# Kernel optimization log

Hardware: AMD Instinct MI355X
Metric: run time of the kernel (lower is better)

The kernel has to match this reference:

```python
import jax, jax.numpy as jnp
import numpy as np

_S = np.float32(1.0 / np.sqrt(2.0))
_lo = np.array([_S, _S], np.float32)   # dec_lo reversed == rec_lo for db1
_hi = np.array([_S, -_S], np.float32)  # dec_hi reversed == rec_hi for db1
# filters[k][i,j]: k=0 LL/2, k=1 hi(i)*lo(j), k=2 lo(i)*hi(j), k=3 hi*hi  (matches torch unsqueeze outer products)
DEC = np.stack([np.outer(_lo, _lo) / 2.0, np.outer(_hi, _lo), np.outer(_lo, _hi), np.outer(_hi, _hi)]).astype(np.float32)
INV = np.stack([np.outer(_lo, _lo) * 2.0, np.outer(_hi, _lo), np.outer(_lo, _hi), np.outer(_hi, _hi)]).astype(np.float32)
INV_FLIP = np.ascontiguousarray(INV[:, ::-1, ::-1])  # spatially flipped for conv_transpose-as-dilated-conv

DN = ('NCHW', 'OIHW', 'NCHW')


def wt(x):
    # single grouped (depthwise x4) strided conv == per-channel loop in the original
    N, C, H, W = x.shape
    k = jnp.broadcast_to(jnp.asarray(DEC)[None], (C, 4, 2, 2)).reshape(C * 4, 1, 2, 2)
    r = jax.lax.conv_general_dilated(x, k, (2, 2), 'VALID', dimension_numbers=DN, feature_group_count=C)
    r = r.reshape(N, C, 4, H // 2, W // 2)
    r = jnp.concatenate([r[:, :, :1], (r[:, :, 1:] + 1.0) / 2.0], axis=2)  # detail remap
    return r.reshape(N, 4 * C, H // 2, W // 2)


def iwt(v):
    N, C4, H, W = v.shape
    C = C4 // 4
    r = v.reshape(N, C, 4, H, W)
    r = jnp.concatenate([r[:, :, :1], 2.0 * r[:, :, 1:] - 1.0], axis=2).reshape(N, C4, H, W)
    k = jnp.broadcast_to(jnp.asarray(INV_FLIP)[None], (C, 4, 2, 2))
    # conv_transpose2d(stride=2, k=2) == dilated conv with lhs_dilation=2, pad 1, flipped kernel
    return jax.lax.conv_general_dilated(r, k, (1, 1), ((1, 1), (1, 1)), lhs_dilation=(2, 2),
                                        dimension_numbers=DN, feature_group_count=C)


def ws_conv(x, w, b, pad):
    # weight standardization: subtract mean over (in,kh,kw), divide by per-filter std (unbiased) + 1e-5
    wc = w - w.mean(axis=(1, 2, 3), keepdims=True)
    std = wc.reshape(w.shape[0], -1).std(axis=1, ddof=1).reshape(-1, 1, 1, 1) + 1e-5
    y = jax.lax.conv_general_dilated(x, wc / std, (1, 1), ((pad, pad), (pad, pad)), dimension_numbers=DN)
    return y if b is None else y + b[None, :, None, None]


def gn(x, g, b, G):
    N, C, H, W = x.shape
    xr = x.reshape(N, G, -1)
    m = xr.mean(-1, keepdims=True)
    v = xr.var(-1, keepdims=True)
    xr = (xr - m) * jax.lax.rsqrt(v + 1e-5)
    return xr.reshape(N, C, H, W) * g[None, :, None, None] + b[None, :, None, None]


def lrelu(t):
    return jnp.where(t > 0, t, 0.2 * t)


def setup_inputs() -> dict:
    key = jax.random.key(0)
    ks = iter(jax.random.split(key, 32))
    f32 = jnp.float32
    d = {}
    d['x'] = jax.random.normal(next(ks), (16, 3, 256, 256), f32)
    def wgt(shape):
        return 0.05 * jax.random.normal(next(ks), shape, f32)
    def bias(n):
        return 0.01 * jax.random.normal(next(ks), (n,), f32)
    c = 16
    d['conv1_w'], d['conv1_b'] = wgt((c, 12, 3, 3)), bias(c)
    d['conv2_w'], d['conv2_b'] = wgt((4 * c, 4 * c, 3, 3)), bias(4 * c)
    d['conv3_w'], d['conv3_b'] = wgt((16 * c, 16 * c, 3, 3)), bias(16 * c)
    d['conv4_w'], d['conv4_b'] = wgt((64 * c, 64 * c, 3, 3)), bias(64 * c)
    d['convd1_w'], d['convd1_b'] = wgt((12, c, 3, 3)), bias(12)
    d['convd2_w'], d['convd2_b'] = wgt((c, 2 * c, 3, 3)), bias(c)
    d['convd3_w'], d['convd3_b'] = wgt((4 * c, 8 * c, 3, 3)), bias(4 * c)
    d['convd4_w'], d['convd4_b'] = wgt((16 * c, 32 * c, 3, 3)), bias(16 * c)
    d['final_w'] = wgt((2, 3, 1, 1))
    for name, n in (('gn1', c), ('gn2', 4 * c), ('gn3', 16 * c), ('gn4', 64 * c)):
        d[name + '_w'] = 1.0 + 0.1 * jax.random.normal(next(ks), (n,), f32)
        d[name + '_b'] = 0.01 * jax.random.normal(next(ks), (n,), f32)
    return d


def reference(x, conv1_w, conv1_b, conv2_w, conv2_b, conv3_w, conv3_b, conv4_w, conv4_b,
              convd1_w, convd1_b, convd2_w, convd2_b, convd3_w, convd3_b, convd4_w, convd4_b,
              final_w, gn1_w, gn1_b, gn2_w, gn2_b, gn3_w, gn3_b, gn4_w, gn4_b):
    w1 = wt(x)
    c1 = gn(lrelu(ws_conv(w1, conv1_w, conv1_b, 1)), gn1_w, gn1_b, 2)
    w2 = wt(c1)
    c2 = gn(lrelu(ws_conv(w2, conv2_w, conv2_b, 1)), gn2_w, gn2_b, 8)
    w3 = wt(c2)
    c3 = gn(lrelu(ws_conv(w3, conv3_w, conv3_b, 1)), gn3_w, gn3_b, 32)
    w4 = wt(c3)
    c4 = gn(lrelu(ws_conv(w4, conv4_w, conv4_b, 1)), gn4_w, gn4_b, 128)
    c5 = gn(lrelu(ws_conv(c4, conv4_w, conv4_b, 1)), gn4_w, gn4_b, 128)
    c6 = ws_conv(c5, conv4_w, conv4_b, 1)
    ic4 = lrelu(c6 + w4)
    iw4 = jnp.concatenate([c3, iwt(ic4)], axis=1)
    ic3 = gn(lrelu(ws_conv(iw4, convd4_w, convd4_b, 1)), gn3_w, gn3_b, 32)
    iw3 = jnp.concatenate([c2, iwt(ic3)], axis=1)
    ic2 = gn(lrelu(ws_conv(iw3, convd3_w, convd3_b, 1)), gn2_w, gn2_b, 8)
    iw2 = jnp.concatenate([c1, iwt(ic2)], axis=1)
    ic1 = gn(lrelu(ws_conv(iw2, convd2_w, convd2_b, 1)), gn1_w, gn1_b, 2)
    iw1 = lrelu(ws_conv(ic1, convd1_w, convd1_b, 1))
    y = ws_conv(iwt(iw1), final_w, None, 0)
    return y
```

## Files before the change

### kernel.cpp

```cpp
#include <hip/hip_runtime.h>
#include <math.h>


#define NB 16

typedef _Float16 f16;
typedef _Float16 f16x8 __attribute__((ext_vector_type(8)));
typedef _Float16 f16x4 __attribute__((ext_vector_type(4)));
typedef float f32x4 __attribute__((ext_vector_type(4)));
typedef unsigned int u32;

#define LLDS16(gp, lp)                                                          \
  __builtin_amdgcn_global_load_lds((const __attribute__((address_space(1))) u32*)(const void*)(gp), \
                                   (__attribute__((address_space(3))) u32*)(void*)(lp), 16, 0, 0)

__device__ __forceinline__ void ws_reduce(const float* wp, int fan, float* red,
                                          float& mean, float& inv) {
  float s = 0.f, s2 = 0.f;
  for (int i = threadIdx.x; i < fan; i += 256) { float v = wp[i]; s += v; s2 += v * v; }
  red[threadIdx.x] = s; red[256 + threadIdx.x] = s2;
  __syncthreads();
  for (int st = 128; st > 0; st >>= 1) {
    if (threadIdx.x < st) {
      red[threadIdx.x] += red[threadIdx.x + st];
      red[256 + threadIdx.x] += red[256 + threadIdx.x + st];
    }
    __syncthreads();
  }
  float sum = red[0], sumsq = red[256];
  mean = sum / (float)fan;
  float var = (sumsq - sum * mean) / (float)(fan - 1);
  if (var < 0.f) var = 0.f;
  inv = 1.0f / (sqrtf(var) + 1e-5f);
}

__global__ void ws_all_kernel(const float* w0, float* o0, const float* w1, float* o1,
                              const float* w2, float* o2, const float* w3, float* o3) {
  __shared__ float red[512];
  int b = blockIdx.x;
  const float* w; float* o; int fan, oi;
  if (b < 16)      { w = w0; o = o0; fan = 108; oi = b; }
  else if (b < 28) { w = w1; o = o1; fan = 144; oi = b - 16; }
  else if (b < 44) { w = w2; o = o2; fan = 288; oi = b - 28; }
  else             { w = w3; o = o3; fan = 3;   oi = b - 44; }
  const float* wp = w + (size_t)oi * fan;
  float mean, inv; ws_reduce(wp, fan, red, mean, inv);
  for (int i = threadIdx.x; i < fan; i += 256)
    o[(size_t)oi * fan + i] = (wp[i] - mean) * inv;
}

__global__ void ws_f16_all_kernel(const float* w0, f16* o0, const float* w1, f16* o1,
                                  const float* w2, f16* o2, const float* w3, f16* o3,
                                  const float* w4, f16* o4) {
  __shared__ float red[512];
  int b = blockIdx.x;
  const float* w; f16* o; int fan, Cin, Cout, oi;
  if (b < 64)        { w = w0; o = o0; fan = 576;  Cin = 64;   Cout = 64;   oi = b; }
  else if (b < 320)  { w = w1; o = o1; fan = 2304; Cin = 256;  Cout = 256;  oi = b - 64; }
  else if (b < 1344) { w = w2; o = o2; fan = 9216; Cin = 1024; Cout = 1024; oi = b - 320; }
  else if (b < 1408) { w = w3; o = o3; fan = 1152; Cin = 128;  Cout = 64;   oi = b - 1344; }
  else               { w = w4; o = o4; fan = 4608; Cin = 512;  Cout = 256;  oi = b - 1408; }
  const float* wp = w + (size_t)oi * fan;
  float mean, inv; ws_reduce(wp, fan, red, mean, inv);
  for (int i = threadIdx.x; i < fan; i += 256) {
    int ci = i / 9, tap = i - ci * 9;
    o[((size_t)tap * Cout + oi) * Cin + ci] = (f16)((wp[i] - mean) * inv);
  }
}

__device__ __forceinline__ void halo_write(f16* buf, int C, int H, int W, int t) {
  int c8s = C >> 3;
  int c8 = t % c8s; int q = t / c8s;
  int P = 2 * (W + 2) + 2 * H;
  int b = q % P; int n = q / P;
  int y, x;
  if (b < W + 2) { y = 0; x = b; }
  else if (b < 2 * (W + 2)) { y = H + 1; x = b - (W + 2); }
  else { int bb = b - 2 * (W + 2); y = 1 + (bb >> 1); x = (bb & 1) ? (W + 1) : 0; }
  size_t a = (((size_t)n * (H + 2) + y) * (W + 2) + x) * C + c8 * 8;
  *(f16x8*)(buf + a) = (f16x8){0, 0, 0, 0, 0, 0, 0, 0};
}

__global__ void halo2_kernel(f16* b0, int c0, int h0, int w0, int n0,
                             f16* b1, int c1, int h1, int w1, int total) {
  int idx = blockIdx.x * 256 + threadIdx.x;
  if (idx >= total) return;
  if (idx < n0) halo_write(b0, c0, h0, w0, idx);
  else halo_write(b1, c1, h1, w1, idx - n0);
}

__global__ void zero_halo_kernel(f16* __restrict__ buf, int C, int H, int W, int total8) {
  int idx = blockIdx.x * 256 + threadIdx.x;
  if (idx >= total8) return;
  halo_write(buf, C, H, W, idx);
}

__global__ void wt_kernel(const float* __restrict__ in, float* __restrict__ out,
                          int C, int Ho, int Wo, int total) {
  int idx = blockIdx.x * 256 + threadIdx.x;
  if (idx >= total) return;
  int w = idx % Wo; int t = idx / Wo;
  int h = t % Ho; t /= Ho;
  int c = t % C; int n = t / C;
  int Wi = 2 * Wo;
  const float* ip = in + (((size_t)n * C + c) * (2 * Ho) + 2 * h) * Wi + 2 * w;
  float a = ip[0], b = ip[1], cc = ip[Wi], d = ip[Wi + 1];
  size_t cs = (size_t)Ho * Wo;
  float* op = out + (((size_t)n * 4 * C + 4 * c) * Ho + h) * Wo + w;
  op[0]      = 0.25f * (a + b + cc + d);
  op[cs]     = 0.25f * (a + b - cc - d) + 0.5f;
  op[2 * cs] = 0.25f * (a - b + cc - d) + 0.5f;
  op[3 * cs] = 0.25f * (a - b - cc + d) + 0.5f;
}

__global__ void concat_iwt_kernel(const float* __restrict__ skip, const float* __restrict__ v,
                                  float* __restrict__ out, const float* __restrict__ gnp,
                                  const float* __restrict__ gamma, const float* __restrict__ beta,
                                  int G, int Sg, int len, int C, int Hh, int Wh,
                                  int totalA, int total) {
  int idx = blockIdx.x * 256 + threadIdx.x;
  if (idx >= total) return;
  int W = 2 * Wh, H = 2 * Hh; int HWs = H * W;
  if (idx < totalA) {
    int p = idx % HWs; int t = idx / HWs; int c = t % C; int n = t / C;
    out[((size_t)n * 2 * C + c) * HWs + p] = skip[idx];
    return;
  }
  int i2 = idx - totalA;
  int w = i2 % Wh; int t = i2 / Wh; int h = t % Hh; t /= Hh;
  int c = t % C; int n = t / C;
  size_t cs = (size_t)Hh * Wh;
  const float* vp = v + (((size_t)n * 4 * C + 4 * c) * Hh + h) * Wh + w;
  float v0 = vp[0], v1 = vp[cs], v2 = vp[2 * cs], v3 = vp[3 * cs];
  if (gnp) {
    int cpg = (4 * C) / G;
    int g = (4 * c) / cpg;
    const float* pp = gnp + (size_t)((n * G + g) * Sg) * 2;
    float s = 0.f, s2 = 0.f;
    for (int i = 0; i < Sg; ++i) { s += pp[2 * i]; s2 += pp[2 * i + 1]; }
    float mean = s / (float)len;
    float var = s2 / (float)len - mean * mean;
    if (var < 0.f) var = 0.f;
    float inv = rsqrtf(var + 1e-5f);
    v0 = (v0 - mean) * inv * gamma[4 * c]     + beta[4 * c];
    v1 = (v1 - mean) * inv * gamma[4 * c + 1] + beta[4 * c + 1];
    v2 = (v2 - mean) * inv * gamma[4 * c + 2] + beta[4 * c + 2];
    v3 = (v3 - mean) * inv * gamma[4 * c + 3] + beta[4 * c + 3];
  }
  v1 = 2.f * v1 - 1.f; v2 = 2.f * v2 - 1.f; v3 = 2.f * v3 - 1.f;
  float* op = out + (((size_t)n * 2 * C + C + c) * H + 2 * h) * (size_t)W + 2 * w;
  op[0]     = v0 + 0.5f * ( v1 + v2 + v3);
  op[1]     = v0 + 0.5f * ( v1 - v2 - v3);
  op[W]     = v0 + 0.5f * (-v1 + v2 - v3);
  op[W + 1] = v0 + 0.5f * (-v1 - v2 + v3);
}

__global__ __launch_bounds__(256) void to_nhwc_pad_kernel(const float* __restrict__ in,
                                                          f16* __restrict__ out,
                                                          int C, int H, int W) {
  __shared__ f16 sm[32][264];
  int HW = H * W;
  int p0 = blockIdx.x * 256, c0 = blockIdx.y * 32, n = blockIdx.z;
  int t = threadIdx.x;
  const float* ip = in + ((size_t)n * C + c0) * HW + p0;
#pragma unroll 8
  for (int r = 0; r < 32; ++r) sm[r][t] = (f16)ip[(size_t)r * HW + t];
  __syncthreads();
#pragma unroll
  for (int i = 0; i < 4; ++i) {
    int c = t + i * 256;
    int pl = c >> 2, cio = (c & 3) * 8;
    f16x8 v;
#pragma unroll
    for (int u = 0; u < 8; ++u) v[u] = sm[cio + u][pl];
    int p = p0 + pl; int y = p / W; int x = p - y * W;
    *(f16x8*)(out + (((size_t)n * (H + 2) + y + 1) * (W + 2) + x + 1) * C + c0 + cio) = v;
  }
}

__global__ __launch_bounds__(256) void gn_nhwc_kernel(
    const float* __restrict__ in, const float* __restrict__ gnp,
    const float* __restrict__ gamma, const float* __restrict__ beta,
    f16* __restrict__ out, int C, int H, int W, int G, int Sg, int len) {
  __shared__ f16 sm[32][264];
  int HW = H * W;
  int p0 = blockIdx.x * 256, c0 = blockIdx.y * 32, n = blockIdx.z;
  int t = threadIdx.x;
  int cpg = C / G;
  const float* ip = in + ((size_t)n * C + c0) * HW + p0;
#pragma unroll 8
  for (int r = 0; r < 32; ++r) {
    int c = c0 + r; int g = c / cpg;
    const float* pp = gnp + (size_t)((n * G + g) * Sg) * 2;
    float s = 0.f, s2 = 0.f;
    for (int i = 0; i < Sg; ++i) { s += pp[2 * i]; s2 += pp[2 * i + 1]; }
    float mean = s / (float)len;
    float var = s2 / (float)len - mean * mean;
    if (var < 0.f) var = 0.f;
    float inv = rsqrtf(var + 1e-5f);
    float ga = gamma[c], be = beta[c];
    sm[r][t] = (f16)((ip[(size_t)r * HW + t] - mean) * inv * ga + be);
  }
  __syncthreads();
#pragma unroll
  for (int i = 0; i < 4; ++i) {
    int c = t + i * 256;
    int pl = c >> 2, cio = (c & 3) * 8;
    f16x8 v;
#pragma unroll
    for (int u = 0; u < 8; ++u) v[u] = sm[cio + u][pl];
    int p = p0 + pl; int y = p / W; int x = p - y * W;
    *(f16x8*)(out + (((size_t)n * (H + 2) + y + 1) * (W + 2) + x + 1) * C + c0 + cio) = v;
  }
}

__global__ void iwt_final_kernel(const float* __restrict__ v, const float* __restrict__ w,
                                 float* __restrict__ out, int total) {
  int idx = blockIdx.x * 256 + threadIdx.x;
  if (idx >= total) return;
  int ww = idx % 128; int t = idx / 128;
  int hh = t % 128; int n = t / 128;
  size_t cs = (size_t)128 * 128;
  float y0[3], y1[3], y2[3], y3[3];
#pragma unroll
  for (int c = 0; c < 3; ++c) {
    const float* vp = v + ((size_t)n * 12 + 4 * c) * cs + (size_t)hh * 128 + ww;
    float v0 = vp[0];
    float v1 = 2.f * vp[cs] - 1.f, v2 = 2.f * vp[2 * cs] - 1.f, v3 = 2.f * vp[3 * cs] - 1.f;
    y0[c] = v0 + 0.5f * ( v1 + v2 + v3);
    y1[c] = v0 + 0.5f * ( v1 - v2 - v3);
    y2[c] = v0 + 0.5f * (-v1 + v2 - v3);
    y3[c] = v0 + 0.5f * (-v1 - v2 + v3);
  }
  float w0 = w[0], w1 = w[1], w2 = w[2], w3 = w[3], w4 = w[4], w5 = w[5];
  size_t ocs = (size_t)256 * 256;
  float* o0 = out + (size_t)n * 2 * ocs + (size_t)(2 * hh) * 256 + 2 * ww;
  o0[0]   = w0 * y0[0] + w1 * y0[1] + w2 * y0[2];
  o0[1]   = w0 * y1[0] + w1 * y1[1] + w2 * y1[2];
  o0[256] = w0 * y2[0] + w1 * y2[1] + w2 * y2[2];
  o0[257] = w0 * y3[0] + w1 * y3[1] + w2 * y3[2];
  float* o1 = o0 + ocs;
  o1[0]   = w3 * y0[0] + w4 * y0[1] + w5 * y0[2];
  o1[1]   = w3 * y1[0] + w4 * y1[1] + w5 * y1[2];
  o1[256] = w3 * y2[0] + w4 * y2[1] + w5 * y2[2];
  o1[257] = w3 * y3[0] + w4 * y3[1] + w5 * y3[2];
}

__global__ __launch_bounds__(256) void conv_mfma6_kernel(
    const f16* __restrict__ A, const f16* __restrict__ Wp,
    f16* __restrict__ part, int Cin, int H, int W, int Cout, int HW) {
  constexpr int CH = 128 * 64;
  __shared__ f16 Asm[2 * CH];
  __shared__ f16 Bsm[2 * CH];

  const int tid = threadIdx.x;
  const int w = tid >> 6, lane = tid & 63;
  const int m0 = blockIdx.x * 128;
  const int co0 = blockIdx.y * 128;
  const int Wp2 = W + 2;

  const f16* gA[4]; const f16* gB[4];
  int lOff[4];
#pragma unroll
  for (int e = 0; e < 4; ++e) {
    int c = e * 256 + tid;
    int r = c >> 3, j = c & 7;
    int jx = j ^ (r & 7);
    int m = m0 + r; int n = m / HW; int p = m - n * HW;
    int y = p / W; int x = p - y * W;
    gA[e] = A + (((size_t)n * (H + 2) + y + 1) * Wp2 + (x + 1)) * Cin + jx * 8;
    gB[e] = Wp + (size_t)(co0 + r) * Cin + jx * 8;
    lOff[e] = (e * 256 + w * 64) * 8;
  }

  const int wm = w & 1, wn = w >> 1;
  const int lr = lane & 15, quad = lane >> 4;
  int aoffs[4][2], boffs[4][2];
#pragma unroll
  for (int i = 0; i < 4; ++i)
#pragma unroll
    for (int kk = 0; kk < 2; ++kk) {
      int r = wm * 64 + i * 16 + lr;
      int cidx = kk * 4 + quad;
      aoffs[i][kk] = (r * 8 + (cidx ^ (r & 7))) * 8;
      int rb = wn * 64 + i * 16 + lr;
      boffs[i][kk] = (rb * 8 + (cidx ^ (rb & 7))) * 8;
    }

  f32x4 acc[4][4];
#pragma unroll
  for (int i = 0; i < 4; ++i)
#pragma unroll
    for (int j = 0; j < 4; ++j) acc[i][j] = (f32x4){0.f, 0.f, 0.f, 0.f};

  const int kpt = Cin >> 6;
  const int nit = (9 * kpt) / gridDim.z;
  const int it0 = blockIdx.z * nit;
  const size_t bstride = (size_t)Cout * Cin;

  auto stageAB = [&](int it, int sel) {
    int tap = it / kpt, kk = it - tap * kpt;
    int dy = tap / 3 - 1, dx = tap % 3 - 1;
    long offA = ((long)dy * Wp2 + dx) * Cin + (kk << 6);
    long offB = (long)tap * bstride + (kk << 6);
    f16* ab = Asm + sel * CH;
    f16* bb = Bsm + sel * CH;
#pragma unroll
    for (int e = 0; e < 4; ++e) {
      LLDS16(gA[e] + offA, ab + lOff[e]);
      LLDS16(gB[e] + offB, bb + lOff[e]);
    }
  };

  stageAB(it0, 0);
  int sel = 0;
  for (int ii = 0; ii < nit; ++ii) {
    __syncthreads();
    if (ii + 1 < nit) stageAB(it0 + ii + 1, sel ^ 1);
    const f16* ab = Asm + sel * CH;
    const f16* bb = Bsm + sel * CH;
    f16x8 af[4][2], bf[4][2];
#pragma unroll
    for (int i = 0; i < 4; ++i)
#pragma unroll
      for (int kk = 0; kk < 2; ++kk) {
        af[i][kk] = *(const f16x8*)&ab[aoffs[i][kk]];
        bf[i][kk] = *(const f16x8*)&bb[boffs[i][kk]];
      }
#pragma unroll
    for (int kk = 0; kk < 2; ++kk)
#pragma unroll
      for (int i = 0; i < 4; ++i)
#pragma unroll
        for (int j = 0; j < 4; ++j)
          acc[i][j] = __builtin_amdgcn_mfma_f32_16x16x32_f16(af[i][kk], bf[j][kk], acc[i][j], 0, 0, 0);
    sel ^= 1;
  }

  const size_t pbase = (size_t)blockIdx.z * NB * Cout * HW;
#pragma unroll
  for (int i = 0; i < 4; ++i) {
    int mg = m0 + wm * 64 + i * 16 + quad * 4;
    int n = mg / HW, p = mg - n * HW;
#pragma unroll
    for (int j = 0; j < 4; ++j) {
      int co = co0 + wn * 64 + j * 16 + lr;
      f32x4 v = acc[i][j];
      f16x4 h;
#pragma unroll
      for (int r = 0; r < 4; ++r) h[r] = (f16)v[r];
      *(f16x4*)&part[pbase + ((size_t)n * Cout + co) * HW + p] = h;
    }
  }
}

__global__ __launch_bounds__(256) void reduceS_kernel(
    const f16* __restrict__ part, const float* __restrict__ bias,
    const float* __restrict__ add, float* __restrict__ out,
    int Cout, int HW, int S, int do_lrelu, int total4,
    float* __restrict__ gnp, int G, int Sg) {
  __shared__ float red[512];
  int idx = blockIdx.x * 256 + threadIdx.x;
  if (idx >= total4) return;
  size_t sstride = (size_t)NB * Cout * HW;
  int hw4 = HW >> 2;
  int p4 = idx % hw4; int t = idx / hw4;
  int c = t % Cout;
  size_t eoff = (size_t)t * HW + p4 * 4;
  float b = bias[c];
  f32x4 o = {b, b, b, b};
  for (int s = 0; s < S; ++s) {
    f16x4 a = *(const f16x4*)(part + s * sstride + eoff);
#pragma unroll
    for (int r = 0; r < 4; ++r) o[r] += (float)a[r];
  }
  if (add) {
    f32x4 av = *(const f32x4*)(add + eoff);
#pragma unroll
    for (int r = 0; r < 4; ++r) o[r] += av[r];
  }
  if (do_lrelu)
#pragma unroll
    for (int r = 0; r < 4; ++r) o[r] = o[r] > 0.f ? o[r] : 0.2f * o[r];
  *(f32x4*)(out + eoff) = o;
  if (gnp) {
    float ls = o[0] + o[1] + o[2] + o[3];
    float ls2 = o[0]*o[0] + o[1]*o[1] + o[2]*o[2] + o[3]*o[3];
    red[threadIdx.x] = ls; red[256 + threadIdx.x] = ls2;
    __syncthreads();
    for (int st = 128; st > 0; st >>= 1) {
      if (threadIdx.x < st) {
        red[threadIdx.x] += red[threadIdx.x + st];
        red[256 + threadIdx.x] += red[256 + threadIdx.x + st];
      }
      __syncthreads();
    }
    if (threadIdx.x == 0) {
      int flat0 = blockIdx.x * 1024;
      int chw = Cout * HW;
      int n = flat0 / chw;
      int rem = flat0 - n * chw;
      int L = (Cout / G) * HW;
      int g = rem / L;
      int s = (rem - g * L) >> 10;
      gnp[((n * G + g) * Sg + s) * 2] = red[0];
      gnp[((n * G + g) * Sg + s) * 2 + 1] = red[256];
    }
  }
}

__global__ __launch_bounds__(256) void conv_mfma2_kernel(
    const f16* __restrict__ A, const f16* __restrict__ Wp,
    const float* __restrict__ bias, float* __restrict__ out,
    int Cin, int H, int W, int Cout, int HW, int do_lrelu) {
  constexpr int BM = 128, BN = 64, BK = 64;
  __shared__ f16 Asm[BM * BK];
  __shared__ f16 Bsm[BN * BK];

  const int tid = threadIdx.x;
  const int w = tid >> 6, lane = tid & 63;
  const int m0 = blockIdx.x * BM;
  const int co0 = blockIdx.y * BN;
  const int Wp2 = W + 2;

  const f16* gA[4];
  int lAoff[4];
#pragma unroll
  for (int e = 0; e < 4; ++e) {
    int c = e * 256 + tid;
    int r = c >> 3, j = c & 7;
    int jx = j ^ (r & 7);
    int m = m0 + r; int n = m / HW; int p = m - n * HW;
    int y = p / W; int x = p - y * W;
    gA[e] = A + (((size_t)n * (H + 2) + y + 1) * Wp2 + (x + 1)) * Cin + jx * 8;
    lAoff[e] = (e * 256 + w * 64) * 8;
  }
  const f16* gB[2];
  int lBoff[2];
#pragma unroll
  for (int e = 0; e < 2; ++e) {
    int c = e * 256 + tid;
    int r = c >> 3, j = c & 7;
    int jx = j ^ (r & 7);
    gB[e] = Wp + (size_t)(co0 + r) * Cin + jx * 8;
    lBoff[e] = (e * 256 + w * 64) * 8;
  }

  const int wm = w & 1, wn = w >> 1;
  const int lr = lane & 15, quad = lane >> 4;
  int aoffs[4][2], boffs[2][2];
#pragma unroll
  for (int i = 0; i < 4; ++i)
#pragma unroll
    for (int kk = 0; kk < 2; ++kk) {
      int r = wm * 64 + i * 16 + lr;
      int cidx = kk * 4 + quad;
      aoffs[i][kk] = (r * 8 + (cidx ^ (r & 7))) * 8;
    }
#pragma unroll
  for (int jn = 0; jn < 2; ++jn)
#pragma unroll
    for (int kk = 0; kk < 2; ++kk) {
      int rb = wn * 32 + jn * 16 + lr;
      int cidx = kk * 4 + quad;
      boffs[jn][kk] = (rb * 8 + (cidx ^ (rb & 7))) * 8;
    }

  f32x4 acc[4][2];
#pragma unroll
  for (int i = 0; i < 4; ++i)
#pragma unroll
    for (int jn = 0; jn < 2; ++jn) acc[i][jn] = (f32x4){0.f, 0.f, 0.f, 0.f};

  for (int tap = 0; tap < 9; ++tap) {
    const int dy = tap / 3 - 1, dx = tap % 3 - 1;
    const long tapA = ((long)dy * Wp2 + dx) * Cin;
    const long tapB = (size_t)tap * Cout * Cin;
    for (int kc = 0; kc < Cin; kc += BK) {
      __syncthreads();
#pragma unroll
      for (int e = 0; e < 4; ++e) LLDS16(gA[e] + tapA + kc, Asm + lAoff[e]);
#pragma unroll
      for (int e = 0; e < 2; ++e) LLDS16(gB[e] + tapB + kc, Bsm + lBoff[e]);
      __syncthreads();

      f16x8 af[4][2], bf[2][2];
#pragma unroll
      for (int i = 0; i < 4; ++i)
#pragma unroll
        for (int kk = 0; kk < 2; ++kk) af[i][kk] = *(const f16x8*)&Asm[aoffs[i][kk]];
#pragma unroll
      for (int jn = 0; jn < 2; ++jn)
#pragma unroll
        for (int kk = 0; kk < 2; ++kk) bf[jn][kk] = *(const f16x8*)&Bsm[boffs[jn][kk]];
#pragma unroll
      for (int kk = 0; kk < 2; ++kk)
#pragma unroll
        for (int i = 0; i < 4; ++i)
#pragma unroll
          for (int jn = 0; jn < 2; ++jn)
            acc[i][jn] = __builtin_amdgcn_mfma_f32_16x16x32_f16(af[i][kk], bf[jn][kk], acc[i][jn], 0, 0, 0);
    }
  }

#pragma unroll
  for (int i = 0; i < 4; ++i) {
    int mg = m0 + wm * 64 + i * 16 + quad * 4;
    int n = mg / HW, p = mg - n * HW;
#pragma unroll
    for (int jn = 0; jn < 2; ++jn) {
      int co = co0 + wn * 32 + jn * 16 + lr;
      float b = bias[co];
      f32x4 v = acc[i][jn];
#pragma unroll
      for (int r = 0; r < 4; ++r) {
        float u = v[r] + b;
        v[r] = (do_lrelu && u < 0.f) ? 0.2f * u : u;
      }
      *(f32x4*)&out[((size_t)n * Cout + co) * HW + p] = v;
    }
  }
}

template <int CO, int CIC>
__global__ __launch_bounds__(256) void conv3x3_kernel(
    const float* __restrict__ in, const float* __restrict__ wgt,
    const float* __restrict__ bias, float* __restrict__ out,
    int Cin, int H, int W, int Cout, int do_lrelu, float* __restrict__ gnp) {
  __shared__ float sm[CIC][18][18];
  int tiles_x = W >> 4;
  int bt = blockIdx.x;
  int tx0 = (bt % tiles_x) << 4;
  int ty0 = (bt / tiles_x) << 4;
  int co0 = blockIdx.y * CO;
  int n = blockIdx.z;
  int tid = threadIdx.x;
  int lx = tid & 15, ly = tid >> 4;

  float acc[CO];
#pragma unroll
  for (int i = 0; i < CO; i++) acc[i] = 0.f;

  const float* inb = in + (size_t)n * Cin * H * W;

  for (int ci0 = 0; ci0 < Cin; ci0 += CIC) {
    __syncthreads();
    for (int idx = tid; idx < CIC * 324; idx += 256) {
      int ci = idx / 324;
      int r = idx - ci * 324;
      int gy = r / 18, gx = r - gy * 18;
      int iy = ty0 + gy - 1, ix = tx0 + gx - 1;
      float v = 0.f;
      if ((unsigned)iy < (unsigned)H && (unsigned)ix < (unsigned)W)
        v = inb[((size_t)(ci0 + ci)) * H * W + (size_t)iy * W + ix];
      sm[ci][gy][gx] = v;
    }
    __syncthreads();
#pragma unroll
    for (int ci = 0; ci < CIC; ci++) {
      float x00 = sm[ci][ly][lx],     x01 = sm[ci][ly][lx + 1],     x02 = sm[ci][ly][lx + 2];
      float x10 = sm[ci][ly + 1][lx], x11 = sm[ci][ly + 1][lx + 1], x12 = sm[ci][ly + 1][lx + 2];
      float x20 = sm[ci][ly + 2][lx], x21 = sm[ci][ly + 2][lx + 1], x22 = sm[ci][ly + 2][lx + 2];
      const float* wp = wgt + ((size_t)co0 * Cin + (ci0 + ci)) * 9;
#pragma unroll
      for (int co = 0; co < CO; co++) {
        const float* wc = wp + (size_t)co * Cin * 9;
        float a = acc[co];
        a = fmaf(wc[0], x00, a); a = fmaf(wc[1], x01, a); a = fmaf(wc[2], x02, a);
        a = fmaf(wc[3], x10, a); a = fmaf(wc[4], x11, a); a = fmaf(wc[5], x12, a);
        a = fmaf(wc[6], x20, a); a = fmaf(wc[7], x21, a); a = fmaf(wc[8], x22, a);
        acc[co] = a;
      }
    }
  }

  float vout[CO];
#pragma unroll
  for (int co = 0; co < CO; co++) {
    float v = acc[co] + bias[co0 + co];
    if (do_lrelu) v = v > 0.f ? v : 0.2f * v;
    vout[co] = v;
  }

  if (gnp) {
    float p0 = 0.f, q0 = 0.f, p1 = 0.f, q1 = 0.f;
#pragma unroll
    for (int co = 0; co < 8; ++co) { p0 += vout[co]; q0 += vout[co] * vout[co]; }
#pragma unroll
    for (int co = 8; co < CO; ++co) { p1 += vout[co]; q1 += vout[co] * vout[co]; }
    float* red = &sm[0][0][0];
    __syncthreads();
    red[tid] = p0; red[256 + tid] = q0; red[512 + tid] = p1; red[768 + tid] = q1;
    __syncthreads();
    for (int st = 128; st > 0; st >>= 1) {
      if (tid < st) {
        red[tid] += red[tid + st]; red[256 + tid] += red[256 + tid + st];
        red[512 + tid] += red[512 + tid + st]; red[768 + tid] += red[768 + tid + st];
      }
      __syncthreads();
    }
    if (tid == 0) {
      int S = gridDim.x;
      gnp[((n * 2 + 0) * S + blockIdx.x) * 2]     = red[0];
      gnp[((n * 2 + 0) * S + blockIdx.x) * 2 + 1] = red[256];
      gnp[((n * 2 + 1) * S + blockIdx.x) * 2]     = red[512];
      gnp[((n * 2 + 1) * S + blockIdx.x) * 2 + 1] = red[768];
    }
  }

  int oy = ty0 + ly, ox = tx0 + lx;
#pragma unroll
  for (int co = 0; co < CO; co++)
    out[(((size_t)n * Cout + co0 + co) * H + oy) * W + ox] = vout[co];
}

__global__ __launch_bounds__(256) void gn_stats_kernel(const float* __restrict__ x,
                                                       float* __restrict__ part,
                                                       int C, int HW, int G, int SPLIT) {
  __shared__ float red[512];
  int gs = blockIdx.x;
  int g = gs / SPLIT, s = gs - g * SPLIT;
  int n = blockIdx.y;
  int cpg = C / G;
  int len = cpg * HW;
  int chunk = len / SPLIT;
  size_t base = ((size_t)n * C + (size_t)g * cpg) * HW + (size_t)s * chunk;
  const f32x4* xp = (const f32x4*)(x + base);
  int chunk4 = chunk >> 2;
  float sm = 0.f, s2 = 0.f;
  for (int i = threadIdx.x; i < chunk4; i += 256) {
    f32x4 v = xp[i];
    sm += v.x + v.y + v.z + v.w;
    s2 += v.x * v.x + v.y * v.y + v.z * v.z + v.w * v.w;
  }
  red[threadIdx.x] = sm; red[256 + threadIdx.x] = s2;
  __syncthreads();
  for (int st = 128; st > 0; st >>= 1) {
    if (threadIdx.x < st) {
      red[threadIdx.x] += red[threadIdx.x + st];
      red[256 + threadIdx.x] += red[256 + threadIdx.x + st];
    }
    __syncthreads();
  }
  if (threadIdx.x == 0) {
    int o = ((n * G + g) * SPLIT + s) * 2;
    part[o] = red[0]; part[o + 1] = red[256];
  }
}

__global__ __launch_bounds__(256) void gn_apply_kernel(float* __restrict__ x,
                                                       const float* __restrict__ gnp,
                                                       const float* __restrict__ gamma,
                                                       const float* __restrict__ beta,
                                                       int C, int HW, int G, int Sg, int len,
                                                       int total4) {
  int idx = blockIdx.x * 256 + threadIdx.x;
  if (idx >= total4) return;
  int flat0 = blockIdx.x * 1024;
  int chw = C * HW;
  int n = flat0 / chw;
  int rem = flat0 - n * chw;
  int L = (C / G) * HW;
  int g = rem / L;
  const float* pp = gnp + (size_t)((n * G + g) * Sg) * 2;
  float s = 0.f, s2 = 0.f;
  for (int i = 0; i < Sg; ++i) { s += pp[2 * i]; s2 += pp[2 * i + 1]; }
  float mean = s / (float)len;
  float var = s2 / (float)len - mean * mean;
  if (var < 0.f) var = 0.f;
  float inv = rsqrtf(var + 1e-5f);
  int hw4 = HW >> 2;
  int p4 = idx % hw4; int t = idx / hw4;
  int c = t % C;
  float ga = gamma[c], be = beta[c];
  f32x4* xp = (f32x4*)(x + ((size_t)t * HW)) + p4;
  f32x4 v = *xp;
#pragma unroll
  for (int r = 0; r < 4; ++r) v[r] = (v[r] - mean) * inv * ga + be;
  *xp = v;
}


extern "C" void kernel_launch(void* const* d_in, const int* in_sizes, int n_in,
                              void* d_out, int out_size, void* d_ws, size_t ws_size,
                              hipStream_t stream) {
  const float* x        = (const float*)d_in[0];
  const float* conv1_w  = (const float*)d_in[1];
  const float* conv1_b  = (const float*)d_in[2];
  const float* conv2_w  = (const float*)d_in[3];
  const float* conv2_b  = (const float*)d_in[4];
  const float* conv3_w  = (const float*)d_in[5];
  const float* conv3_b  = (const float*)d_in[6];
  const float* conv4_w  = (const float*)d_in[7];
  const float* conv4_b  = (const float*)d_in[8];
  const float* convd1_w = (const float*)d_in[9];
  const float* convd1_b = (const float*)d_in[10];
  const float* convd2_w = (const float*)d_in[11];
  const float* convd2_b = (const float*)d_in[12];
  const float* convd3_w = (const float*)d_in[13];
  const float* convd3_b = (const float*)d_in[14];
  const float* convd4_w = (const float*)d_in[15];
  const float* convd4_b = (const float*)d_in[16];
  const float* final_w  = (const float*)d_in[17];
  const float* gn1_w = (const float*)d_in[18];
  const float* gn1_b = (const float*)d_in[19];
  const float* gn2_w = (const float*)d_in[20];
  const float* gn2_b = (const float*)d_in[21];
  const float* gn3_w = (const float*)d_in[22];
  const float* gn3_b = (const float*)d_in[23];
  const float* gn4_w = (const float*)d_in[24];
  const float* gn4_b = (const float*)d_in[25];

  char* base = (char*)d_ws;
  size_t off = 0;
  auto allocB = [&](size_t bytes) { size_t o = off; off = (off + bytes + 255) & ~(size_t)255; return o; };

  size_t o_sw1  = allocB(16 * 108 * 4);
  size_t o_swd1 = allocB(12 * 144 * 4);
  size_t o_swd2 = allocB(16 * 288 * 4);
  size_t o_swf  = allocB(6 * 4);
  size_t o_pw2  = allocB((size_t)9 * 64 * 64 * 2);
  size_t o_pw3  = allocB((size_t)9 * 256 * 256 * 2);
  size_t o_pw4  = allocB((size_t)9 * 1024 * 1024 * 2);
  size_t o_pwd3 = allocB((size_t)9 * 64 * 128 * 2);
  size_t o_pwd4 = allocB((size_t)9 * 256 * 512 * 2);
  size_t o_R1   = allocB((size_t)NB * 66 * 66 * 128 * 2);
  size_t o_R2   = allocB((size_t)NB * 34 * 34 * 512 * 2);
  size_t o_gnp  = allocB(16384 * 4);
  size_t o_c1 = allocB((size_t)NB * 16 * 128 * 128 * 4);
  size_t o_c2 = allocB((size_t)NB * 64 * 64 * 64 * 4);
  size_t o_c3 = allocB((size_t)NB * 256 * 32 * 32 * 4);
  size_t o_w4 = allocB((size_t)NB * 1024 * 16 * 16 * 4);
  size_t o_t1 = allocB((size_t)NB * 1024 * 16 * 16 * 4);
  size_t o_t2 = allocB((size_t)NB * 512 * 32 * 32 * 4);

  if (off > ws_size) return;

  float* c1 = (float*)(base + o_c1);
  float* c2 = (float*)(base + o_c2);
  float* c3 = (float*)(base + o_c3);
  float* w4 = (float*)(base + o_w4);
  float* t1 = (float*)(base + o_t1);
  float* t2 = (float*)(base + o_t2);
  f16* part  = (f16*)(base + o_R1);
  f16* ah64  = (f16*)(base + o_R1);
  f16* ah128 = (f16*)(base + o_R1);
  f16* ah256 = (f16*)(base + o_R2);
  f16* ah1k  = (f16*)(base + o_R2);
  f16* ah512 = (f16*)(base + o_R2);
  f16* pw2 = (f16*)(base + o_pw2);
  f16* pw3 = (f16*)(base + o_pw3);
  f16* pw4 = (f16*)(base + o_pw4);
  f16* pwd3 = (f16*)(base + o_pwd3);
  f16* pwd4 = (f16*)(base + o_pwd4);
  float* gnp = (float*)(base + o_gnp);

  {
    int n0 = NB * (2 * 66 + 2 * 64) * (64 / 8);
    int n1 = NB * (2 * 34 + 2 * 32) * (256 / 8);
    int tot = n0 + n1;
    halo2_kernel<<<(tot + 255) / 256, 256, 0, stream>>>(ah64, 64, 64, 64, n0,
                                                        ah256, 256, 32, 32, tot);
  }
  ws_all_kernel<<<46, 256, 0, stream>>>(conv1_w, (float*)(base + o_sw1),
                                        convd1_w, (float*)(base + o_swd1),
                                        convd2_w, (float*)(base + o_swd2),
                                        final_w, (float*)(base + o_swf));
  ws_f16_all_kernel<<<1664, 256, 0, stream>>>(conv2_w, pw2, conv3_w, pw3, conv4_w, pw4,
                                              convd3_w, pwd3, convd4_w, pwd4);

  auto prep_nhwc = [&](const float* in, f16* ah, int C, int H, int W, int zero) {
    if (zero) {
      int total8 = NB * (2 * (W + 2) + 2 * H) * (C / 8);
      zero_halo_kernel<<<(total8 + 255) / 256, 256, 0, stream>>>(ah, C, H, W, total8);
    }
    dim3 g((H * W) / 256, C / 32, NB);
    to_nhwc_pad_kernel<<<g, 256, 0, stream>>>(in, ah, C, H, W);
  };
  auto cm6 = [&](const f16* a, const f16* wt, const float* b, float* dest, const float* add,
                 int Cin, int Hs, int Ws, int Cout, int lr, int G, int Sg) {
    dim3 g((NB * Hs * Ws) / 128, Cout / 128, 2);
    conv_mfma6_kernel<<<g, 256, 0, stream>>>(a, wt, part, Cin, Hs, Ws, Cout, Hs * Ws);
    int total4 = (NB * Cout * Hs * Ws) >> 2;
    reduceS_kernel<<<(total4 + 255) / 256, 256, 0, stream>>>(
        part, b, add, dest, Cout, Hs * Ws, 2, lr, total4, G ? gnp : nullptr, G, Sg);
  };
  auto cm2 = [&](const f16* a, const f16* wt, const float* b, float* o,
                 int Cin, int Hs, int Ws, int Cout, int lr) {
    dim3 g((NB * Hs * Ws) / 128, Cout / 64);
    conv_mfma2_kernel<<<g, 256, 0, stream>>>(a, wt, b, o, Cin, Hs, Ws, Cout, Hs * Ws, lr);
  };
  auto launch_wt = [&](const float* in, float* out, int C, int Ho, int Wo) {
    int total = NB * C * Ho * Wo;
    wt_kernel<<<(total + 255) / 256, 256, 0, stream>>>(in, out, C, Ho, Wo, total);
  };
  auto apply = [&](float* xb, const float* g, const float* b, int C, int HW, int G, int Sg) {
    int len = (C / G) * HW;
    int total4 = (NB * C * HW) >> 2;
    gn_apply_kernel<<<(total4 + 255) / 256, 256, 0, stream>>>(xb, gnp, g, b, C, HW, G, Sg,
                                                              len, total4);
  };
  auto stats = [&](const float* xb, int C, int HW, int G, int SPLIT) {
    dim3 gsd(G * SPLIT, NB);
    gn_stats_kernel<<<gsd, 256, 0, stream>>>(xb, gnp, C, HW, G, SPLIT);
  };
  auto concat_iwt = [&](const float* skip, const float* v, float* out, int C, int Hh, int Wh,
                        const float* gg, const float* gb, int G, int Sg) {
    int totalA = NB * C * 4 * Hh * Wh;
    int total = totalA + NB * C * Hh * Wh;
    int len = G ? ((4 * C) / G) * Hh * Wh : 1;
    concat_iwt_kernel<<<(total + 255) / 256, 256, 0, stream>>>(
        skip, v, out, G ? gnp : nullptr, gg, gb, G, Sg, len, C, Hh, Wh, totalA, total);
  };

  launch_wt(x, t1, 3, 128, 128);
  {
    dim3 g(64, 1, NB);
    conv3x3_kernel<16, 4><<<g, 256, 0, stream>>>(t1, (float*)(base + o_sw1), conv1_b,
                                                 c1, 12, 128, 128, 16, 1, gnp);
  }
  apply(c1, gn1_w, gn1_b, 16, 128 * 128, 2, 64);

  launch_wt(c1, t1, 16, 64, 64);
  prep_nhwc(t1, ah64, 64, 64, 64, 0);
  cm2(ah64, pw2, conv2_b, c2, 64, 64, 64, 64, 1);
  stats(c2, 64, 4096, 8, 16);
  apply(c2, gn2_w, gn2_b, 64, 4096, 8, 16);

  launch_wt(c2, t1, 64, 32, 32);
  prep_nhwc(t1, ah256, 256, 32, 32, 0);
  cm6(ah256, pw3, conv3_b, c3, nullptr, 256, 32, 32, 256, 1, 32, 8);
  apply(c3, gn3_w, gn3_b, 256, 1024, 32, 8);

  launch_wt(c3, w4, 256, 16, 16);
  prep_nhwc(w4, ah1k, 1024, 16, 16, 1);

  cm6(ah1k, pw4, conv4_b, t1, nullptr, 1024, 16, 16, 1024, 1, 128, 2);
  {
    dim3 g(1, 32, NB);
    gn_nhwc_kernel<<<g, 256, 0, stream>>>(t1, gnp, gn4_w, gn4_b, ah1k, 1024, 16, 16,
                                          128, 2, 2048);
  }
  cm6(ah1k, pw4, conv4_b, t2, nullptr, 1024, 16, 16, 1024, 1, 128, 2);
  {
    dim3 g(1, 32, NB);
    gn_nhwc_kernel<<<g, 256, 0, stream>>>(t2, gnp, gn4_w, gn4_b, ah1k, 1024, 16, 16,
                                          128, 2, 2048);
  }
  cm6(ah1k, pw4, conv4_b, t1, w4, 1024, 16, 16, 1024, 1, 0, 0);

  concat_iwt(c3, t1, t2, 256, 16, 16, nullptr, nullptr, 0, 0);
  prep_nhwc(t2, ah512, 512, 32, 32, 1);
  cm6(ah512, pwd4, convd4_b, t1, nullptr, 512, 32, 32, 256, 1, 32, 8);
  concat_iwt(c2, t1, t2, 64, 32, 32, gn3_w, gn3_b, 32, 8);
  prep_nhwc(t2, ah128, 128, 64, 64, 1);
  cm2(ah128, pwd3, convd3_b, t1, 128, 64, 64, 64, 1);
  stats(t1, 64, 4096, 8, 16);
  concat_iwt(c1, t1, t2, 16, 64, 64, gn2_w, gn2_b, 8, 16);
  {
    dim3 g(64, 1, NB);
    conv3x3_kernel<16, 4><<<g, 256, 0, stream>>>(t2, (float*)(base + o_swd2), convd2_b,
                                                 t1, 32, 128, 128, 16, 1, gnp);
  }
  apply(t1, gn1_w, gn1_b, 16, 128 * 128, 2, 64);
  {
    dim3 g(64, 1, NB);
    conv3x3_kernel<12, 4><<<g, 256, 0, stream>>>(t1, (float*)(base + o_swd1), convd1_b,
                                                 t2, 16, 128, 128, 12, 1, nullptr);
  }
  {
    int total = NB * 128 * 128;
    iwt_final_kernel<<<(total + 255) / 256, 256, 0, stream>>>(t2, (float*)(base + o_swf),
                                                              (float*)d_out, total);
  }
}
```

Before: 961.7 us.

## Fuse wavelet transform into NHWC packing, double-buffer small conv, fuse final iwt

Adds a wt_nhwc kernel that computes the Haar decomposition and writes fp16 padded NHWC directly, replacing the separate wt and prep_nhwc passes (with an optional fp32 copy for the residual). Converts the 64-wide MFMA conv into a double-buffered LDS pipeline that prefetches the next K slice while computing the current one. Fuses the last 3x3 conv with the inverse wavelet and final 1x1 mix so the 12-channel intermediate never goes to memory. These changes target memory traffic and launch count, at the cost of more LDS and a halo-zero launch.

```diff
diff --git a/kernel.cpp b/kernel.cpp
--- a/kernel.cpp
+++ b/kernel.cpp
@@ -8,6 +8,7 @@
 typedef _Float16 f16x8 __attribute__((ext_vector_type(8)));
 typedef _Float16 f16x4 __attribute__((ext_vector_type(4)));
 typedef float f32x4 __attribute__((ext_vector_type(4)));
+typedef float f32x2 __attribute__((ext_vector_type(2)));
 typedef unsigned int u32;
 
 #define LLDS16(gp, lp)                                                          \
@@ -111,6 +112,49 @@
   op[cs]     = 0.25f * (a + b - cc - d) + 0.5f;
   op[2 * cs] = 0.25f * (a - b + cc - d) + 0.5f;
   op[3 * cs] = 0.25f * (a - b - cc + d) + 0.5f;
+}
+
+__global__ __launch_bounds__(256) void wt_nhwc_kernel(
+    const float* __restrict__ in, f16* __restrict__ out, float* __restrict__ out32,
+    int C, int Ho, int Wo) {
+  __shared__ f16 sm[32][264];
+  int HWo = Ho * Wo;
+  int p0 = blockIdx.x * 256, c0 = blockIdx.y * 8, n = blockIdx.z;
+  int t = threadIdx.x;
+  int p = p0 + t; int h = p / Wo; int ww = p - h * Wo;
+  int Wi = 2 * Wo;
+  int C4 = 4 * C;
+#pragma unroll
+  for (int r = 0; r < 8; ++r) {
+    const float* ip = in + (((size_t)n * C + c0 + r) * (2 * Ho) + 2 * h) * Wi + 2 * ww;
+    f32x2 u0 = *(const f32x2*)ip;
+    f32x2 u1 = *(const f32x2*)(ip + Wi);
+    float a = u0.x, b = u0.y, cc = u1.x, d = u1.y;
+    float v0 = 0.25f * (a + b + cc + d);
+    float v1 = 0.25f * (a + b - cc - d) + 0.5f;
+    float v2 = 0.25f * (a - b + cc - d) + 0.5f;
+    float v3 = 0.25f * (a - b - cc + d) + 0.5f;
+    sm[4 * r][t]     = (f16)v0;
+    sm[4 * r + 1][t] = (f16)v1;
+    sm[4 * r + 2][t] = (f16)v2;
+    sm[4 * r + 3][t] = (f16)v3;
+    if (out32) {
+      float* op = out32 + (((size_t)n * C4 + 4 * (c0 + r)) * Ho + h) * Wo + ww;
+      size_t cs = (size_t)HWo;
+      op[0] = v0; op[cs] = v1; op[2 * cs] = v2; op[3 * cs] = v3;
+    }
+  }
+  __syncthreads();
+#pragma unroll
+  for (int i = 0; i < 4; ++i) {
+    int c = t + i * 256;
+    int pl = c >> 2, cio = (c & 3) * 8;
+    f16x8 v;
+#pragma unroll
+    for (int u = 0; u < 8; ++u) v[u] = sm[cio + u][pl];
+    int pp = p0 + pl; int y = pp / Wo; int x = pp - y * Wo;
+    *(f16x8*)(out + (((size_t)n * (Ho + 2) + y + 1) * (Wo + 2) + x + 1) * C4 + c0 * 4 + cio) = v;
+  }
 }
 
 __global__ void concat_iwt_kernel(const float* __restrict__ skip, const float* __restrict__ v,
@@ -214,38 +258,6 @@
   }
 }
 
-__global__ void iwt_final_kernel(const float* __restrict__ v, const float* __restrict__ w,
-                                 float* __restrict__ out, int total) {
-  int idx = blockIdx.x * 256 + threadIdx.x;
-  if (idx >= total) return;
-  int ww = idx % 128; int t = idx / 128;
-  int hh = t % 128; int n = t / 128;
-  size_t cs = (size_t)128 * 128;
-  float y0[3], y1[3], y2[3], y3[3];
-#pragma unroll
-  for (int c = 0; c < 3; ++c) {
-    const float* vp = v + ((size_t)n * 12 + 4 * c) * cs + (size_t)hh * 128 + ww;
-    float v0 = vp[0];
-    float v1 = 2.f * vp[cs] - 1.f, v2 = 2.f * vp[2 * cs] - 1.f, v3 = 2.f * vp[3 * cs] - 1.f;
-    y0[c] = v0 + 0.5f * ( v1 + v2 + v3);
-    y1[c] = v0 + 0.5f * ( v1 - v2 - v3);
-    y2[c] = v0 + 0.5f * (-v1 + v2 - v3);
-    y3[c] = v0 + 0.5f * (-v1 - v2 + v3);
-  }
-  float w0 = w[0], w1 = w[1], w2 = w[2], w3 = w[3], w4 = w[4], w5 = w[5];
-  size_t ocs = (size_t)256 * 256;
-  float* o0 = out + (size_t)n * 2 * ocs + (size_t)(2 * hh) * 256 + 2 * ww;
-  o0[0]   = w0 * y0[0] + w1 * y0[1] + w2 * y0[2];
-  o0[1]   = w0 * y1[0] + w1 * y1[1] + w2 * y1[2];
-  o0[256] = w0 * y2[0] + w1 * y2[1] + w2 * y2[2];
-  o0[257] = w0 * y3[0] + w1 * y3[1] + w2 * y3[2];
-  float* o1 = o0 + ocs;
-  o1[0]   = w3 * y0[0] + w4 * y0[1] + w5 * y0[2];
-  o1[1]   = w3 * y1[0] + w4 * y1[1] + w5 * y1[2];
-  o1[256] = w3 * y2[0] + w4 * y2[1] + w5 * y2[2];
-  o1[257] = w3 * y3[0] + w4 * y3[1] + w5 * y3[2];
-}
-
 __global__ __launch_bounds__(256) void conv_mfma6_kernel(
     const f16* __restrict__ A, const f16* __restrict__ Wp,
     f16* __restrict__ part, int Cin, int H, int W, int Cout, int HW) {
@@ -409,18 +421,19 @@
   }
 }
 
-__global__ __launch_bounds__(256) void conv_mfma2_kernel(
+__global__ __launch_bounds__(256) void conv_mfma3_kernel(
     const f16* __restrict__ A, const f16* __restrict__ Wp,
     const float* __restrict__ bias, float* __restrict__ out,
     int Cin, int H, int W, int Cout, int HW, int do_lrelu) {
-  constexpr int BM = 128, BN = 64, BK = 64;
-  __shared__ f16 Asm[BM * BK];
-  __shared__ f16 Bsm[BN * BK];
+  constexpr int CHA = 128 * 64;
+  constexpr int CHB = 64 * 64;
+  __shared__ f16 Asm[2 * CHA];
+  __shared__ f16 Bsm[2 * CHB];
 
   const int tid = threadIdx.x;
   const int w = tid >> 6, lane = tid & 63;
-  const int m0 = blockIdx.x * BM;
-  const int co0 = blockIdx.y * BN;
+  const int m0 = blockIdx.x * 128;
+  const int co0 = blockIdx.y * 64;
   const int Wp2 = W + 2;
 
   const f16* gA[4];
@@ -472,35 +485,47 @@
 #pragma unroll
     for (int jn = 0; jn < 2; ++jn) acc[i][jn] = (f32x4){0.f, 0.f, 0.f, 0.f};
 
-  for (int tap = 0; tap < 9; ++tap) {
-    const int dy = tap / 3 - 1, dx = tap % 3 - 1;
-    const long tapA = ((long)dy * Wp2 + dx) * Cin;
-    const long tapB = (size_t)tap * Cout * Cin;
-    for (int kc = 0; kc < Cin; kc += BK) {
-      __syncthreads();
-#pragma unroll
-      for (int e = 0; e < 4; ++e) LLDS16(gA[e] + tapA + kc, Asm + lAoff[e]);
-#pragma unroll
-      for (int e = 0; e < 2; ++e) LLDS16(gB[e] + tapB + kc, Bsm + lBoff[e]);
-      __syncthreads();
-
-      f16x8 af[4][2], bf[2][2];
+  const int kpt = Cin >> 6;
+  const int nit = 9 * kpt;
+  const size_t bstride = (size_t)Cout * Cin;
+
+  auto stageAB = [&](int it, int sel) {
+    int tap = it / kpt, kk = it - tap * kpt;
+    int dy = tap / 3 - 1, dx = tap % 3 - 1;
+    long offA = ((long)dy * Wp2 + dx) * Cin + (kk << 6);
+    long offB = (long)tap * bstride + (kk << 6);
+    f16* ab = Asm + sel * CHA;
+    f16* bb = Bsm + sel * CHB;
+#pragma unroll
+    for (int e = 0; e < 4; ++e) LLDS16(gA[e] + offA, ab + lAoff[e]);
+#pragma unroll
+    for (int e = 0; e < 2; ++e) LLDS16(gB[e] + offB, bb + lBoff[e]);
+  };
+
+  stageAB(0, 0);
+  int sel = 0;
+  for (int ii = 0; ii < nit; ++ii) {
+    __syncthreads();
+    if (ii + 1 < nit) stageAB(ii + 1, sel ^ 1);
+    const f16* ab = Asm + sel * CHA;
+    const f16* bb = Bsm + sel * CHB;
+    f16x8 af[4][2], bf[2][2];
+#pragma unroll
+    for (int i = 0; i < 4; ++i)
+#pragma unroll
+      for (int kk = 0; kk < 2; ++kk) af[i][kk] = *(const f16x8*)&ab[aoffs[i][kk]];
+#pragma unroll
+    for (int jn = 0; jn < 2; ++jn)
+#pragma unroll
+      for (int kk = 0; kk < 2; ++kk) bf[jn][kk] = *(const f16x8*)&bb[boffs[jn][kk]];
+#pragma unroll
+    for (int kk = 0; kk < 2; ++kk)
 #pragma unroll
       for (int i = 0; i < 4; ++i)
 #pragma unroll
-        for (int kk = 0; kk < 2; ++kk) af[i][kk] = *(const f16x8*)&Asm[aoffs[i][kk]];
-#pragma unroll
-      for (int jn = 0; jn < 2; ++jn)
-#pragma unroll
-        for (int kk = 0; kk < 2; ++kk) bf[jn][kk] = *(const f16x8*)&Bsm[boffs[jn][kk]];
-#pragma unroll
-      for (int kk = 0; kk < 2; ++kk)
-#pragma unroll
-        for (int i = 0; i < 4; ++i)
-#pragma unroll
-          for (int jn = 0; jn < 2; ++jn)
-            acc[i][jn] = __builtin_amdgcn_mfma_f32_16x16x32_f16(af[i][kk], bf[jn][kk], acc[i][jn], 0, 0, 0);
-    }
+        for (int jn = 0; jn < 2; ++jn)
+          acc[i][jn] = __builtin_amdgcn_mfma_f32_16x16x32_f16(af[i][kk], bf[jn][kk], acc[i][jn], 0, 0, 0);
+    sel ^= 1;
   }
 
 #pragma unroll
@@ -612,6 +637,92 @@
 #pragma unroll
   for (int co = 0; co < CO; co++)
     out[(((size_t)n * Cout + co0 + co) * H + oy) * W + ox] = vout[co];
+}
+
+template <int CO, int CIC>
+__global__ __launch_bounds__(256) void conv3x3_iwt_kernel(
+    const float* __restrict__ in, const float* __restrict__ wgt,
+    const float* __restrict__ bias, const float* __restrict__ fw,
+    float* __restrict__ out, int Cin, int H, int W) {
+  __shared__ float sm[CIC][18][18];
+  int tiles_x = W >> 4;
+  int bt = blockIdx.x;
+  int tx0 = (bt % tiles_x) << 4;
+  int ty0 = (bt / tiles_x) << 4;
+  int n = blockIdx.z;
+  int tid = threadIdx.x;
+  int lx = tid & 15, ly = tid >> 4;
+
+  float acc[CO];
+#pragma unroll
+  for (int i = 0; i < CO; i++) acc[i] = 0.f;
+
+  const float* inb = in + (size_t)n * Cin * H * W;
+
+  for (int ci0 = 0; ci0 < Cin; ci0 += CIC) {
+    __syncthreads();
+    for (int idx = tid; idx < CIC * 324; idx += 256) {
+      int ci = idx / 324;
+      int r = idx - ci * 324;
+      int gy = r / 18, gx = r - gy * 18;
+      int iy = ty0 + gy - 1, ix = tx0 + gx - 1;
+      float v = 0.f;
+      if ((unsigned)iy < (unsigned)H && (unsigned)ix < (unsigned)W)
+        v = inb[((size_t)(ci0 + ci)) * H * W + (size_t)iy * W + ix];
+      sm[ci][gy][gx] = v;
+    }
+    __syncthreads();
+#pragma unroll
+    for (int ci = 0; ci < CIC; ci++) {
+      float x00 = sm[ci][ly][lx],     x01 = sm[ci][ly][lx + 1],     x02 = sm[ci][ly][lx + 2];
+      float x10 = sm[ci][ly + 1][lx], x11 = sm[ci][ly + 1][lx + 1], x12 = sm[ci][ly + 1][lx + 2];
+      float x20 = sm[ci][ly + 2][lx], x21 = sm[ci][ly + 2][lx + 1], x22 = sm[ci][ly + 2][lx + 2];
+      const float* wp = wgt + (size_t)(ci0 + ci) * 9;
+#pragma unroll
+      for (int co = 0; co < CO; co++) {
+        const float* wc = wp + (size_t)co * Cin * 9;
+        float a = acc[co];
+        a = fmaf(wc[0], x00, a); a = fmaf(wc[1], x01, a); a = fmaf(wc[2], x02, a);
+        a = fmaf(wc[3], x10, a); a = fmaf(wc[4], x11, a); a = fmaf(wc[5], x12, a);
+        a = fmaf(wc[6], x20, a); a = fmaf(wc[7], x21, a); a = fmaf(wc[8], x22, a);
+        acc[co] = a;
+      }
+    }
+  }
+
+  float vout[CO];
+#pragma unroll
+  for (int co = 0; co < CO; co++) {
+    float v = acc[co] + bias[co];
+    vout[co] = v > 0.f ? v : 0.2f * v;
+  }
+
+  float y0[3], y1[3], y2[3], y3[3];
+#pragma unroll
+  for (int c = 0; c < 3; ++c) {
+    float v0 = vout[4 * c];
+    float v1 = 2.f * vout[4 * c + 1] - 1.f;
+    float v2 = 2.f * vout[4 * c + 2] - 1.f;
+    float v3 = 2.f * vout[4 * c + 3] - 1.f;
+    y0[c] = v0 + 0.5f * ( v1 + v2 + v3);
+    y1[c] = v0 + 0.5f * ( v1 - v2 - v3);
+    y2[c] = v0 + 0.5f * (-v1 + v2 - v3);
+    y3[c] = v0 + 0.5f * (-v1 - v2 + v3);
+  }
+  float w0 = fw[0], w1 = fw[1], w2 = fw[2], w3 = fw[3], w4 = fw[4], w5 = fw[5];
+  int oy = ty0 + ly, ox = tx0 + lx;
+  int OW = 2 * W;
+  size_t ocs = (size_t)(2 * H) * OW;
+  float* o0 = out + (size_t)n * 2 * ocs + (size_t)(2 * oy) * OW + 2 * ox;
+  o0[0]      = w0 * y0[0] + w1 * y0[1] + w2 * y0[2];
+  o0[1]      = w0 * y1[0] + w1 * y1[1] + w2 * y1[2];
+  o0[OW]     = w0 * y2[0] + w1 * y2[1] + w2 * y2[2];
+  o0[OW + 1] = w0 * y3[0] + w1 * y3[1] + w2 * y3[2];
+  float* o1 = o0 + ocs;
+  o1[0]      = w3 * y0[0] + w4 * y0[1] + w5 * y0[2];
+  o1[1]      = w3 * y1[0] + w4 * y1[1] + w5 * y1[2];
+  o1[OW]     = w3 * y2[0] + w4 * y2[1] + w5 * y2[2];
+  o1[OW + 1] = w3 * y3[0] + w4 * y3[1] + w5 * y3[2];
 }
 
 __global__ __launch_bounds__(256) void gn_stats_kernel(const float* __restrict__ x,
@@ -777,6 +888,10 @@
     dim3 g((H * W) / 256, C / 32, NB);
     to_nhwc_pad_kernel<<<g, 256, 0, stream>>>(in, ah, C, H, W);
   };
+  auto wt_nhwc = [&](const float* in, f16* ah, float* copy32, int C, int Ho, int Wo) {
+    dim3 g((Ho * Wo) / 256, C / 8, NB);
+    wt_nhwc_kernel<<<g, 256, 0, stream>>>(in, ah, copy32, C, Ho, Wo);
+  };
   auto cm6 = [&](const f16* a, const f16* wt, const float* b, float* dest, const float* add,
                  int Cin, int Hs, int Ws, int Cout, int lr, int G, int Sg) {
     dim3 g((NB * Hs * Ws) / 128, Cout / 128, 2);
@@ -785,14 +900,10 @@
     reduceS_kernel<<<(total4 + 255) / 256, 256, 0, stream>>>(
         part, b, add, dest, Cout, Hs * Ws, 2, lr, total4, G ? gnp : nullptr, G, Sg);
   };
-  auto cm2 = [&](const f16* a, const f16* wt, const float* b, float* o,
+  auto cm3 = [&](const f16* a, const f16* wt, const float* b, float* o,
                  int Cin, int Hs, int Ws, int Cout, int lr) {
     dim3 g((NB * Hs * Ws) / 128, Cout / 64);
-    conv_mfma2_kernel<<<g, 256, 0, stream>>>(a, wt, b, o, Cin, Hs, Ws, Cout, Hs * Ws, lr);
-  };
-  auto launch_wt = [&](const float* in, float* out, int C, int Ho, int Wo) {
-    int total = NB * C * Ho * Wo;
-    wt_kernel<<<(total + 255) / 256, 256, 0, stream>>>(in, out, C, Ho, Wo, total);
+    conv_mfma3_kernel<<<g, 256, 0, stream>>>(a, wt, b, o, Cin, Hs, Ws, Cout, Hs * Ws, lr);
   };
   auto apply = [&](float* xb, const float* g, const float* b, int C, int HW, int G, int Sg) {
     int len = (C / G) * HW;
@@ -813,7 +924,10 @@
         skip, v, out, G ? gnp : nullptr, gg, gb, G, Sg, len, C, Hh, Wh, totalA, total);
   };
 
-  launch_wt(x, t1, 3, 128, 128);
+  {
+    int total = NB * 3 * 128 * 128;
+    wt_kernel<<<(total + 255) / 256, 256, 0, stream>>>(x, t1, 3, 128, 128, total);
+  }
   {
     dim3 g(64, 1, NB);
     conv3x3_kernel<16, 4><<<g, 256, 0, stream>>>(t1, (float*)(base + o_sw1), conv1_b,
@@ -821,19 +935,20 @@
   }
   apply(c1, gn1_w, gn1_b, 16, 128 * 128, 2, 64);
 
-  launch_wt(c1, t1, 16, 64, 64);
-  prep_nhwc(t1, ah64, 64, 64, 64, 0);
-  cm2(ah64, pw2, conv2_b, c2, 64, 64, 64, 64, 1);
+  wt_nhwc(c1, ah64, nullptr, 16, 64, 64);
+  cm3(ah64, pw2, conv2_b, c2, 64, 64, 64, 64, 1);
   stats(c2, 64, 4096, 8, 16);
   apply(c2, gn2_w, gn2_b, 64, 4096, 8, 16);
 
-  launch_wt(c2, t1, 64, 32, 32);
-  prep_nhwc(t1, ah256, 256, 32, 32, 0);
+  wt_nhwc(c2, ah256, nullptr, 64, 32, 32);
   cm6(ah256, pw3, conv3_b, c3, nullptr, 256, 32, 32, 256, 1, 32, 8);
   apply(c3, gn3_w, gn3_b, 256, 1024, 32, 8);
 
-  launch_wt(c3, w4, 256, 16, 16);
-  prep_nhwc(w4, ah1k, 1024, 16, 16, 1);
+  {
+    int total8 = NB * (2 * 18 + 2 * 16) * (1024 / 8);
+    zero_halo_kernel<<<(total8 + 255) / 256, 256, 0, stream>>>(ah1k, 1024, 16, 16, total8);
+  }
+  wt_nhwc(c3, ah1k, w4, 256, 16, 16);
 
   cm6(ah1k, pw4, conv4_b, t1, nullptr, 1024, 16, 16, 1024, 1, 128, 2);
   {
@@ -854,7 +969,7 @@
   cm6(ah512, pwd4, convd4_b, t1, nullptr, 512, 32, 32, 256, 1, 32, 8);
   concat_iwt(c2, t1, t2, 64, 32, 32, gn3_w, gn3_b, 32, 8);
   prep_nhwc(t2, ah128, 128, 64, 64, 1);
-  cm2(ah128, pwd3, convd3_b, t1, 128, 64, 64, 64, 1);
+  cm3(ah128, pwd3, convd3_b, t1, 128, 64, 64, 64, 1);
   stats(t1, 64, 4096, 8, 16);
   concat_iwt(c1, t1, t2, 16, 64, 64, gn2_w, gn2_b, 8, 16);
   {
@@ -865,12 +980,8 @@
   apply(t1, gn1_w, gn1_b, 16, 128 * 128, 2, 64);
   {
     dim3 g(64, 1, NB);
-    conv3x3_kernel<12, 4><<<g, 256, 0, stream>>>(t1, (float*)(base + o_swd1), convd1_b,
-                                                 t2, 16, 128, 128, 12, 1, nullptr);
-  }
-  {
-    int total = NB * 128 * 128;
-    iwt_final_kernel<<<(total + 255) / 256, 256, 0, stream>>>(t2, (float*)(base + o_swf),
-                                                              (float*)d_out, total);
-  }
-}
+    conv3x3_iwt_kernel<12, 4><<<g, 256, 0, stream>>>(t1, (float*)(base + o_swd1), convd1_b,
+                                                     (float*)(base + o_swf), (float*)d_out,
+                                                     16, 128, 128);
+  }
+}
```

Result: faster. 921.5 us (-4.2%).
